# Kernel optimization log

Measured on AMD Instinct MI355X. Metric: run time of the kernel, lower is better.

Reference implementation:

```python
import jax, jax.numpy as jnp
import numpy as np

EMBED = 1024
HEADS = 16
HEAD_DIM = EMBED // HEADS
OUT_DIM = 1024


def setup_inputs() -> dict:
    key = jax.random.key(0)
    ks = jax.random.split(key, 8)
    N, L = 2, 2048
    values = jax.random.normal(ks[0], (N, L, EMBED), dtype=jnp.float32)
    keys_t = jax.random.normal(ks[1], (N, L, EMBED), dtype=jnp.float32)
    query = jax.random.normal(ks[2], (N, L, EMBED), dtype=jnp.float32)
    s = 1.0 / np.sqrt(HEAD_DIM)
    Wv = jax.random.normal(ks[3], (HEAD_DIM, HEAD_DIM), dtype=jnp.float32) * s
    Wk = jax.random.normal(ks[4], (HEAD_DIM, HEAD_DIM), dtype=jnp.float32) * s
    Wq = jax.random.normal(ks[5], (HEAD_DIM, HEAD_DIM), dtype=jnp.float32) * s
    Wout = jax.random.normal(ks[6], (OUT_DIM, EMBED), dtype=jnp.float32) * (1.0 / np.sqrt(EMBED))
    bout = jax.random.normal(ks[7], (OUT_DIM,), dtype=jnp.float32) * 0.01
    return {"values": values, "keys": keys_t, "query": query,
            "Wv": Wv, "Wk": Wk, "Wq": Wq, "Wout": Wout, "bout": bout}


def reference(values, keys, query, Wv, Wk, Wq, Wout, bout):
    N, Lq, _ = query.shape
    Lk = keys.shape[1]
    # split into heads: (N, L, H, D)
    v = values.reshape(N, Lk, HEADS, HEAD_DIM)
    k = keys.reshape(N, Lk, HEADS, HEAD_DIM)
    q = query.reshape(N, Lq, HEADS, HEAD_DIM)
    # per-head shared linear projections (torch Linear: x @ W.T, no bias)
    v = jnp.einsum('nlhd,ed->nlhe', v, Wv)
    k = jnp.einsum('nlhd,ed->nlhe', k, Wk)
    q = jnp.einsum('nqhd,ed->nqhe', q, Wq)
    # scores (N, H, Q, K); NOTE: scale is 1/sqrt(embed_size), per original code
    scores = jnp.einsum('nqhd,nkhd->nhqk', q, k) / jnp.sqrt(jnp.float32(EMBED))
    attn = jax.nn.softmax(scores, axis=-1)
    out = jnp.einsum('nhqk,nkhd->nqhd', attn, v).reshape(N, Lq, EMBED)
    # fc_out: x @ Wout.T + bout
    return out @ Wout.T + bout
```

## Files before the change

### kernel.cpp

```cpp
#include <hip/hip_runtime.h>
#include <cstdint>

typedef __attribute__((ext_vector_type(8))) short short8;
typedef __attribute__((ext_vector_type(4))) float floatx4;

#define DEV __device__ __forceinline__

constexpr int NB = 2, Lseq = 2048, NH = 16, HD = 64, EMB = 1024;
constexpr float QSCALE = 0.03125f * 1.4426950408889634f;

DEV uint16_t f2bf(float f) {
  uint32_t x = __builtin_bit_cast(uint32_t, f);
  x += 0x7fffu + ((x >> 16) & 1u);
  return (uint16_t)(x >> 16);
}

DEV uint32_t pack2(float lo, float hi) {
  uint32_t a = __builtin_bit_cast(uint32_t, lo) + 0x8000u;
  uint32_t b = __builtin_bit_cast(uint32_t, hi) + 0x8000u;
  return __builtin_amdgcn_perm(b, a, 0x07060302);
}

DEV void gl_lds16(const void* g, void* l) {
  __builtin_amdgcn_global_load_lds((const __attribute__((address_space(1))) void*)g,
                                   (__attribute__((address_space(3))) void*)l, 16, 0, 0);
}

__global__ __launch_bounds__(256) void cvt_wout_kernel(const float* __restrict__ W,
                                                       uint16_t* __restrict__ Wb) {
  int idx = blockIdx.x * 256 + threadIdx.x;
  float4 v = ((const float4*)W)[idx];
  uint2 p;
  p.x = pack2(v.x, v.y);
  p.y = pack2(v.z, v.w);
  ((uint2*)Wb)[idx] = p;
}

__global__ __launch_bounds__(256) void proj_qk_kernel(
    const float* __restrict__ query, const float* __restrict__ keysrc,
    const float* __restrict__ Wq, const float* __restrict__ Wk,
    uint16_t* __restrict__ qp, uint16_t* __restrict__ kp) {
  __shared__ float xs[64 * 64];
  __shared__ float wl[64 * 68];
  const int t = threadIdx.x;
  const int r0 = blockIdx.x * 64;
  const int group = t >> 6, e = t & 63;

  for (int mat = 0; mat < 2; ++mat) {
    const float* src = mat ? keysrc : query;
    const float* W   = mat ? Wk : Wq;
    uint16_t* dst    = mat ? kp : qp;
    const float sc   = mat ? 1.0f : QSCALE;
    if (mat) __syncthreads();
#pragma unroll
    for (int i = 0; i < 16; ++i) {
      int idx = i * 256 + t;
      wl[(idx >> 6) * 68 + (idx & 63)] = W[idx];
    }
    const float4* s4 = (const float4*)(src + (size_t)r0 * 64);
    float4* x4 = (float4*)xs;
#pragma unroll
    for (int i = 0; i < 4; ++i) x4[i * 256 + t] = s4[i * 256 + t];
    __syncthreads();

    float acc[16];
#pragma unroll
    for (int i = 0; i < 16; ++i) acc[i] = 0.f;
#pragma unroll
    for (int d4 = 0; d4 < 16; ++d4) {
      float4 wv = *(const float4*)(&wl[e * 68 + d4 * 4]);
#pragma unroll
      for (int i = 0; i < 16; ++i) {
        float4 xv = *(const float4*)(&xs[(group * 16 + i) * 64 + d4 * 4]);
        acc[i] += xv.x * wv.x + xv.y * wv.y + xv.z * wv.z + xv.w * wv.w;
      }
    }
#pragma unroll
    for (int i = 0; i < 16; ++i) {
      int r = r0 + group * 16 + i;
      int h = r & 15, l = (r >> 4) & 2047, n = r >> 15;
      dst[(((n * 16 + h) * 2048) + l) * 64 + e] = f2bf(acc[i] * sc);
    }
  }
}

__global__ __launch_bounds__(256) void proj_v_kernel(const float* __restrict__ values,
                                                     const float* __restrict__ Wv,
                                                     uint16_t* __restrict__ vp) {
  __shared__ float xs[64 * 68];
  __shared__ float wl[64 * 68];
  const int t = threadIdx.x;
  const int nh = blockIdx.y, n = nh >> 4, h = nh & 15;
  const int l0 = blockIdx.x * 64;
#pragma unroll
  for (int i = 0; i < 16; ++i) {
    int idx = i * 256 + t;
    wl[(idx >> 6) * 68 + (idx & 63)] = Wv[idx];
  }
  const float4* s4 = (const float4*)values;
#pragma unroll
  for (int i = 0; i < 4; ++i) {
    int idx = i * 256 + t;
    int row = idx >> 4, c = idx & 15;
    *(float4*)(&xs[row * 68 + c * 4]) = s4[(size_t)(n * 2048 + l0 + row) * 256 + h * 16 + c];
  }
  __syncthreads();
  const int e0 = (t >> 6) * 16, lane = t & 63;
  float acc[16];
#pragma unroll
  for (int i = 0; i < 16; ++i) acc[i] = 0.f;
#pragma unroll
  for (int d4 = 0; d4 < 16; ++d4) {
    float4 xv = *(const float4*)(&xs[lane * 68 + d4 * 4]);
#pragma unroll
    for (int i = 0; i < 16; ++i) {
      float4 wv = *(const float4*)(&wl[(e0 + i) * 68 + d4 * 4]);
      acc[i] += xv.x * wv.x + xv.y * wv.y + xv.z * wv.z + xv.w * wv.w;
    }
  }
#pragma unroll
  for (int i = 0; i < 16; ++i)
    vp[((size_t)nh * 64 + e0 + i) * 2048 + l0 + lane] = f2bf(acc[i]);
}

__global__ __launch_bounds__(256) void flash_kernel(const uint16_t* __restrict__ qp,
                                                    const uint16_t* __restrict__ kp,
                                                    const uint16_t* __restrict__ vp,
                                                    uint16_t* __restrict__ xatt) {
  __shared__ uint16_t Kt[2][64 * 64];
  __shared__ uint16_t Vt[2][64 * 64];
  __shared__ uint16_t Pt[4][32 * 72];
  const int t = threadIdx.x;
  const int w = t >> 6, lane = t & 63, quad = lane >> 4, l16 = lane & 15;
  const int nh = blockIdx.y;
  const int q0 = blockIdx.x * 128 + w * 32;
  const uint16_t* Qb = qp + (size_t)nh * Lseq * HD;
  const uint16_t* Kb = kp + (size_t)nh * Lseq * HD;
  const uint16_t* Vb = vp + (size_t)nh * HD * Lseq;
  const int srow = lane >> 3, sc8 = (lane & 7) ^ (lane >> 3);

  short8 bq[2][2];
#pragma unroll
  for (int qb = 0; qb < 2; ++qb) {
    bq[qb][0] = *(const short8*)(Qb + (q0 + qb * 16 + l16) * 64 + quad * 8);
    bq[qb][1] = *(const short8*)(Qb + (q0 + qb * 16 + l16) * 64 + 32 + quad * 8);
  }

  floatx4 o[4][2];
  float psum[2] = {0.f, 0.f};
#pragma unroll
  for (int i = 0; i < 4; ++i)
#pragma unroll
    for (int qb = 0; qb < 2; ++qb) o[i][qb] = floatx4{0.f, 0.f, 0.f, 0.f};

#pragma unroll
  for (int i = 0; i < 2; ++i) {
    int r0 = w * 16 + i * 8;
    gl_lds16(Kb + (r0 + srow) * 64 + sc8 * 8, &Kt[0][r0 * 64]);
    gl_lds16(Vb + (size_t)(r0 + srow) * Lseq + sc8 * 8, &Vt[0][r0 * 64]);
  }

  for (int kb = 0; kb < Lseq / 64; ++kb) {
    __syncthreads();
    const int cur = kb & 1;
    if (kb + 1 < Lseq / 64) {
      const int nxt = cur ^ 1;
      const uint16_t* kg = Kb + (kb + 1) * (64 * 64);
#pragma unroll
      for (int i = 0; i < 2; ++i) {
        int r0 = w * 16 + i * 8;
        gl_lds16(kg + (r0 + srow) * 64 + sc8 * 8, &Kt[nxt][r0 * 64]);
        gl_lds16(Vb + (size_t)(r0 + srow) * Lseq + (kb + 1) * 64 + sc8 * 8, &Vt[nxt][r0 * 64]);
      }
    }

    floatx4 s[4][2];
#pragma unroll
    for (int kb16 = 0; kb16 < 4; ++kb16)
#pragma unroll
      for (int qb = 0; qb < 2; ++qb) s[kb16][qb] = floatx4{0.f, 0.f, 0.f, 0.f};
#pragma unroll
    for (int dc = 0; dc < 2; ++dc) {
#pragma unroll
      for (int kb16 = 0; kb16 < 4; ++kb16) {
        int row = kb16 * 16 + l16;
        short8 ak = *(const short8*)(&Kt[cur][row * 64 + ((dc * 4 + quad) ^ (row & 7)) * 8]);
        s[kb16][0] = __builtin_amdgcn_mfma_f32_16x16x32_bf16(ak, bq[0][dc], s[kb16][0], 0, 0, 0);
        s[kb16][1] = __builtin_amdgcn_mfma_f32_16x16x32_bf16(ak, bq[1][dc], s[kb16][1], 0, 0, 0);
      }
    }

#pragma unroll
    for (int qb = 0; qb < 2; ++qb) {
      uint16_t* pw = &Pt[w][(qb * 16 + l16) * 72];
#pragma unroll
      for (int kb16 = 0; kb16 < 4; ++kb16) {
        float p0 = __builtin_amdgcn_exp2f(s[kb16][qb][0]);
        float p1 = __builtin_amdgcn_exp2f(s[kb16][qb][1]);
        float p2 = __builtin_amdgcn_exp2f(s[kb16][qb][2]);
        float p3 = __builtin_amdgcn_exp2f(s[kb16][qb][3]);
        psum[qb] += (p0 + p1) + (p2 + p3);
        uint2 pk;
        pk.x = pack2(p0, p1);
        pk.y = pack2(p2, p3);
        *(uint2*)(pw + kb16 * 16 + quad * 4) = pk;
      }
    }

    short8 bp[2][2];
#pragma unroll
    for (int qb = 0; qb < 2; ++qb)
#pragma unroll
      for (int kc = 0; kc < 2; ++kc)
        bp[qb][kc] = *(const short8*)(&Pt[w][(qb * 16 + l16) * 72 + kc * 32 + quad * 8]);
#pragma unroll
    for (int kc = 0; kc < 2; ++kc) {
#pragma unroll
      for (int db = 0; db < 4; ++db) {
        int row = db * 16 + l16;
        short8 av = *(const short8*)(&Vt[cur][row * 64 + ((kc * 4 + quad) ^ (row & 7)) * 8]);
        o[db][0] = __builtin_amdgcn_mfma_f32_16x16x32_bf16(av, bp[0][kc], o[db][0], 0, 0, 0);
        o[db][1] = __builtin_amdgcn_mfma_f32_16x16x32_bf16(av, bp[1][kc], o[db][1], 0, 0, 0);
      }
    }
  }

  const int n = nh >> 4, h = nh & 15;
#pragma unroll
  for (int qb = 0; qb < 2; ++qb) {
    float l = psum[qb];
    l += __shfl_xor(l, 16, 64);
    l += __shfl_xor(l, 32, 64);
    float inv = 1.f / l;
    size_t rowb = (size_t)(n * Lseq + q0 + qb * 16 + l16) * EMB + h * 64;
#pragma unroll
    for (int db = 0; db < 4; ++db) {
      uint2 pk;
      pk.x = pack2(o[db][qb][0] * inv, o[db][qb][1] * inv);
      pk.y = pack2(o[db][qb][2] * inv, o[db][qb][3] * inv);
      *(uint2*)(xatt + rowb + db * 16 + quad * 4) = pk;
    }
  }
}

__global__ __launch_bounds__(256) void gemm_out_kernel(const uint16_t* __restrict__ X,
                                                       const uint16_t* __restrict__ Wb,
                                                       const float* __restrict__ bias,
                                                       float* __restrict__ out) {
  __shared__ uint16_t Xt[2][128 * 64];
  __shared__ uint16_t Wt[2][64 * 64];
  const int t = threadIdx.x, w = t >> 6, lane = t & 63, quad = lane >> 4, l16 = lane & 15;
  const int m0 = blockIdx.x * 128, o0 = blockIdx.y * 64;
  const int srow = lane >> 3, sc8 = (lane & 7) ^ (lane >> 3);
  floatx4 c[2][4];
#pragma unroll
  for (int i = 0; i < 2; ++i)
#pragma unroll
    for (int j = 0; j < 4; ++j) c[i][j] = floatx4{0.f, 0.f, 0.f, 0.f};

#pragma unroll
  for (int i = 0; i < 4; ++i) {
    int r0 = w * 32 + i * 8;
    gl_lds16(X + (size_t)(m0 + r0 + srow) * 1024 + sc8 * 8, &Xt[0][r0 * 64]);
  }
#pragma unroll
  for (int i = 0; i < 2; ++i) {
    int r0 = w * 16 + i * 8;
    gl_lds16(Wb + (size_t)(o0 + r0 + srow) * 1024 + sc8 * 8, &Wt[0][r0 * 64]);
  }

  for (int kt = 0; kt < 16; ++kt) {
    __syncthreads();
    const int cur = kt & 1;
    if (kt + 1 < 16) {
      const int nxt = cur ^ 1;
      const int e0 = (kt + 1) * 64;
#pragma unroll
      for (int i = 0; i < 4; ++i) {
        int r0 = w * 32 + i * 8;
        gl_lds16(X + (size_t)(m0 + r0 + srow) * 1024 + e0 + sc8 * 8, &Xt[nxt][r0 * 64]);
      }
#pragma unroll
      for (int i = 0; i < 2; ++i) {
        int r0 = w * 16 + i * 8;
        gl_lds16(Wb + (size_t)(o0 + r0 + srow) * 1024 + e0 + sc8 * 8, &Wt[nxt][r0 * 64]);
      }
    }
#pragma unroll
    for (int kc = 0; kc < 2; ++kc) {
      short8 a[2], b[4];
#pragma unroll
      for (int mf = 0; mf < 2; ++mf) {
        int row = w * 32 + mf * 16 + l16;
        a[mf] = *(const short8*)(&Xt[cur][row * 64 + ((kc * 4 + quad) ^ (row & 7)) * 8]);
      }
#pragma unroll
      for (int nf = 0; nf < 4; ++nf) {
        int rw = nf * 16 + l16;
        b[nf] = *(const short8*)(&Wt[cur][rw * 64 + ((kc * 4 + quad) ^ (rw & 7)) * 8]);
      }
#pragma unroll
      for (int mf = 0; mf < 2; ++mf)
#pragma unroll
        for (int nf = 0; nf < 4; ++nf)
          c[mf][nf] = __builtin_amdgcn_mfma_f32_16x16x32_bf16(a[mf], b[nf], c[mf][nf], 0, 0, 0);
    }
  }
#pragma unroll
  for (int nf = 0; nf < 4; ++nf) {
    float bv = bias[o0 + nf * 16 + l16];
#pragma unroll
    for (int mf = 0; mf < 2; ++mf)
#pragma unroll
      for (int r = 0; r < 4; ++r)
        out[(size_t)(m0 + w * 32 + mf * 16 + quad * 4 + r) * 1024 + o0 + nf * 16 + l16] =
            c[mf][nf][r] + bv;
  }
}

extern "C" void kernel_launch(void* const* d_in, const int* in_sizes, int n_in,
                              void* d_out, int out_size, void* d_ws, size_t ws_size,
                              hipStream_t stream) {
  const float* values = (const float*)d_in[0];
  const float* keys   = (const float*)d_in[1];
  const float* query  = (const float*)d_in[2];
  const float* Wv     = (const float*)d_in[3];
  const float* Wk     = (const float*)d_in[4];
  const float* Wq     = (const float*)d_in[5];
  const float* Wout   = (const float*)d_in[6];
  const float* bout   = (const float*)d_in[7];
  float* out = (float*)d_out;

  uint16_t* ws  = (uint16_t*)d_ws;
  uint16_t* qp  = ws;
  uint16_t* kp  = ws + (size_t)4194304;
  uint16_t* vp  = ws + (size_t)2 * 4194304;
  uint16_t* xat = ws + (size_t)3 * 4194304;
  uint16_t* wbf = ws + (size_t)4 * 4194304;

  cvt_wout_kernel<<<dim3(1024), dim3(256), 0, stream>>>(Wout, wbf);
  proj_qk_kernel<<<dim3(1024), dim3(256), 0, stream>>>(query, keys, Wq, Wk, qp, kp);
  proj_v_kernel<<<dim3(32, 32), dim3(256), 0, stream>>>(values, Wv, vp);
  flash_kernel<<<dim3(16, 32), dim3(256), 0, stream>>>(qp, kp, vp, xat);
  gemm_out_kernel<<<dim3(32, 16), dim3(256), 0, stream>>>(xat, wbf, bout, out);
}
```

Before: 209.7 us.

## Fuse projections and Wout conversion into one MFMA-based prep kernel

Replaces the three preprocessing kernels (Wout bf16 conversion, Q/K projection, V projection) with a single launch where each wavefront independently handles one 64-row tile. The scalar FP32 FMA loops through LDS are replaced by bf16 MFMA 16x16x32 instructions, with inputs loaded straight from global memory into registers and converted on the fly. This cuts two kernel launches and the LDS staging and synchronisation. In exchange the projection inputs are rounded to bf16 before the multiply, which lowers precision, and the per-element 2-byte scattered stores may coalesce less well.

```diff
diff --git a/kernel.cpp b/kernel.cpp
--- a/kernel.cpp
+++ b/kernel.cpp
@@ -26,101 +26,111 @@
                                    (__attribute__((address_space(3))) void*)l, 16, 0, 0);
 }
 
-__global__ __launch_bounds__(256) void cvt_wout_kernel(const float* __restrict__ W,
-                                                       uint16_t* __restrict__ Wb) {
-  int idx = blockIdx.x * 256 + threadIdx.x;
-  float4 v = ((const float4*)W)[idx];
-  uint2 p;
-  p.x = pack2(v.x, v.y);
-  p.y = pack2(v.z, v.w);
-  ((uint2*)Wb)[idx] = p;
-}
-
-__global__ __launch_bounds__(256) void proj_qk_kernel(
-    const float* __restrict__ query, const float* __restrict__ keysrc,
-    const float* __restrict__ Wq, const float* __restrict__ Wk,
-    uint16_t* __restrict__ qp, uint16_t* __restrict__ kp) {
-  __shared__ float xs[64 * 64];
-  __shared__ float wl[64 * 68];
-  const int t = threadIdx.x;
-  const int r0 = blockIdx.x * 64;
-  const int group = t >> 6, e = t & 63;
-
-  for (int mat = 0; mat < 2; ++mat) {
+DEV short8 ld8bf(const float* p, float sc) {
+  float4 u = *(const float4*)p;
+  float4 v = *(const float4*)(p + 4);
+  union { short8 s; uint32_t d[4]; } r;
+  r.d[0] = pack2(u.x * sc, u.y * sc);
+  r.d[1] = pack2(u.z * sc, u.w * sc);
+  r.d[2] = pack2(v.x * sc, v.y * sc);
+  r.d[3] = pack2(v.z * sc, v.w * sc);
+  return r.s;
+}
+
+__global__ __launch_bounds__(256) void prep_kernel(
+    const float* __restrict__ values, const float* __restrict__ keysrc,
+    const float* __restrict__ query, const float* __restrict__ Wv,
+    const float* __restrict__ Wk, const float* __restrict__ Wq,
+    const float* __restrict__ Wout,
+    uint16_t* __restrict__ qp, uint16_t* __restrict__ kp,
+    uint16_t* __restrict__ vp, uint16_t* __restrict__ wbf) {
+  const int t = threadIdx.x, w = t >> 6, lane = t & 63;
+  const int quad = lane >> 4, l16 = lane & 15;
+  const int wid = blockIdx.x * 4 + w;
+  const int mat = wid >> 10, sub = wid & 1023;
+
+  if (mat == 3) {
+#pragma unroll
+    for (int i = 0; i < 4; ++i) {
+      int idx = sub * 256 + i * 64 + lane;
+      float4 v = ((const float4*)Wout)[idx];
+      uint2 p;
+      p.x = pack2(v.x, v.y);
+      p.y = pack2(v.z, v.w);
+      ((uint2*)wbf)[idx] = p;
+    }
+    return;
+  }
+
+  floatx4 c[4][4];
+#pragma unroll
+  for (int i = 0; i < 4; ++i)
+#pragma unroll
+    for (int j = 0; j < 4; ++j) c[i][j] = floatx4{0.f, 0.f, 0.f, 0.f};
+
+  if (mat < 2) {
     const float* src = mat ? keysrc : query;
     const float* W   = mat ? Wk : Wq;
+    const float bsc  = mat ? 1.f : QSCALE;
     uint16_t* dst    = mat ? kp : qp;
-    const float sc   = mat ? 1.0f : QSCALE;
-    if (mat) __syncthreads();
-#pragma unroll
-    for (int i = 0; i < 16; ++i) {
-      int idx = i * 256 + t;
-      wl[(idx >> 6) * 68 + (idx & 63)] = W[idx];
-    }
-    const float4* s4 = (const float4*)(src + (size_t)r0 * 64);
-    float4* x4 = (float4*)xs;
-#pragma unroll
-    for (int i = 0; i < 4; ++i) x4[i * 256 + t] = s4[i * 256 + t];
-    __syncthreads();
-
-    float acc[16];
-#pragma unroll
-    for (int i = 0; i < 16; ++i) acc[i] = 0.f;
-#pragma unroll
-    for (int d4 = 0; d4 < 16; ++d4) {
-      float4 wv = *(const float4*)(&wl[e * 68 + d4 * 4]);
-#pragma unroll
-      for (int i = 0; i < 16; ++i) {
-        float4 xv = *(const float4*)(&xs[(group * 16 + i) * 64 + d4 * 4]);
-        acc[i] += xv.x * wv.x + xv.y * wv.y + xv.z * wv.z + xv.w * wv.w;
-      }
-    }
-#pragma unroll
-    for (int i = 0; i < 16; ++i) {
-      int r = r0 + group * 16 + i;
-      int h = r & 15, l = (r >> 4) & 2047, n = r >> 15;
-      dst[(((n * 16 + h) * 2048) + l) * 64 + e] = f2bf(acc[i] * sc);
-    }
-  }
-}
-
-__global__ __launch_bounds__(256) void proj_v_kernel(const float* __restrict__ values,
-                                                     const float* __restrict__ Wv,
-                                                     uint16_t* __restrict__ vp) {
-  __shared__ float xs[64 * 68];
-  __shared__ float wl[64 * 68];
-  const int t = threadIdx.x;
-  const int nh = blockIdx.y, n = nh >> 4, h = nh & 15;
-  const int l0 = blockIdx.x * 64;
-#pragma unroll
-  for (int i = 0; i < 16; ++i) {
-    int idx = i * 256 + t;
-    wl[(idx >> 6) * 68 + (idx & 63)] = Wv[idx];
-  }
-  const float4* s4 = (const float4*)values;
-#pragma unroll
-  for (int i = 0; i < 4; ++i) {
-    int idx = i * 256 + t;
-    int row = idx >> 4, c = idx & 15;
-    *(float4*)(&xs[row * 68 + c * 4]) = s4[(size_t)(n * 2048 + l0 + row) * 256 + h * 16 + c];
-  }
-  __syncthreads();
-  const int e0 = (t >> 6) * 16, lane = t & 63;
-  float acc[16];
-#pragma unroll
-  for (int i = 0; i < 16; ++i) acc[i] = 0.f;
-#pragma unroll
-  for (int d4 = 0; d4 < 16; ++d4) {
-    float4 xv = *(const float4*)(&xs[lane * 68 + d4 * 4]);
-#pragma unroll
-    for (int i = 0; i < 16; ++i) {
-      float4 wv = *(const float4*)(&wl[(e0 + i) * 68 + d4 * 4]);
-      acc[i] += xv.x * wv.x + xv.y * wv.y + xv.z * wv.z + xv.w * wv.w;
-    }
-  }
-#pragma unroll
-  for (int i = 0; i < 16; ++i)
-    vp[((size_t)nh * 64 + e0 + i) * 2048 + l0 + lane] = f2bf(acc[i]);
+    const int R0 = sub * 64;
+    short8 a[4][2], b[4][2];
+#pragma unroll
+    for (int dc = 0; dc < 2; ++dc) {
+#pragma unroll
+      for (int f = 0; f < 4; ++f) {
+        a[f][dc] = ld8bf(src + (size_t)(R0 + f * 16 + l16) * 64 + dc * 32 + quad * 8, 1.f);
+        b[f][dc] = ld8bf(W + (size_t)(f * 16 + l16) * 64 + dc * 32 + quad * 8, bsc);
+      }
+    }
+#pragma unroll
+    for (int dc = 0; dc < 2; ++dc)
+#pragma unroll
+      for (int mf = 0; mf < 4; ++mf)
+#pragma unroll
+        for (int nf = 0; nf < 4; ++nf)
+          c[mf][nf] = __builtin_amdgcn_mfma_f32_16x16x32_bf16(a[mf][dc], b[nf][dc], c[mf][nf], 0, 0, 0);
+#pragma unroll
+    for (int mf = 0; mf < 4; ++mf) {
+#pragma unroll
+      for (int rr = 0; rr < 4; ++rr) {
+        int r = R0 + mf * 16 + quad * 4 + rr;
+        int h = r & 15, l = (r >> 4) & 2047, n = r >> 15;
+        uint16_t* drow = dst + ((size_t)(n * 16 + h) * 2048 + l) * 64;
+#pragma unroll
+        for (int nf = 0; nf < 4; ++nf) drow[nf * 16 + l16] = f2bf(c[mf][nf][rr]);
+      }
+    }
+  } else {
+    const int nh = sub >> 5, L0 = (sub & 31) * 64;
+    const int n = nh >> 4, h = nh & 15;
+    short8 a[4][2], b[4][2];
+#pragma unroll
+    for (int dc = 0; dc < 2; ++dc) {
+#pragma unroll
+      for (int f = 0; f < 4; ++f) {
+        a[f][dc] = ld8bf(Wv + (size_t)(f * 16 + l16) * 64 + dc * 32 + quad * 8, 1.f);
+        b[f][dc] = ld8bf(values + (size_t)(n * 2048 + L0 + f * 16 + l16) * 1024 + h * 64 + dc * 32 + quad * 8, 1.f);
+      }
+    }
+#pragma unroll
+    for (int dc = 0; dc < 2; ++dc)
+#pragma unroll
+      for (int mf = 0; mf < 4; ++mf)
+#pragma unroll
+        for (int nf = 0; nf < 4; ++nf)
+          c[mf][nf] = __builtin_amdgcn_mfma_f32_16x16x32_bf16(a[mf][dc], b[nf][dc], c[mf][nf], 0, 0, 0);
+#pragma unroll
+    for (int mf = 0; mf < 4; ++mf) {
+#pragma unroll
+      for (int rr = 0; rr < 4; ++rr) {
+        int d = mf * 16 + quad * 4 + rr;
+        uint16_t* drow = vp + ((size_t)nh * 64 + d) * 2048 + L0;
+#pragma unroll
+        for (int nf = 0; nf < 4; ++nf) drow[nf * 16 + l16] = f2bf(c[mf][nf][rr]);
+      }
+    }
+  }
 }
 
 __global__ __launch_bounds__(256) void flash_kernel(const uint16_t* __restrict__ qp,
@@ -338,9 +348,8 @@
   uint16_t* xat = ws + (size_t)3 * 4194304;
   uint16_t* wbf = ws + (size_t)4 * 4194304;
 
-  cvt_wout_kernel<<<dim3(1024), dim3(256), 0, stream>>>(Wout, wbf);
-  proj_qk_kernel<<<dim3(1024), dim3(256), 0, stream>>>(query, keys, Wq, Wk, qp, kp);
-  proj_v_kernel<<<dim3(32, 32), dim3(256), 0, stream>>>(values, Wv, vp);
+  prep_kernel<<<dim3(1024), dim3(256), 0, stream>>>(values, keys, query, Wv, Wk, Wq, Wout,
+                                                    qp, kp, vp, wbf);
   flash_kernel<<<dim3(16, 32), dim3(256), 0, stream>>>(qp, kp, vp, xat);
   gemm_out_kernel<<<dim3(32, 16), dim3(256), 0, stream>>>(xat, wbf, bout, out);
 }
```

Measured after the change: 187.4 us. 1.12x faster.
